# Kernel tuning notes

Measured on AMD Instinct MI355X. Metric: run time of the kernel, lower is better.

## Reference

```python
import jax, jax.numpy as jnp
import numpy as np

B, T, E, H, L, Q, FF, V, C = 4, 2048, 16, 4, 2, 16, 64, 32000, 16
D = E // H  # head_dim = 4


def pos_encoding(t, e):
    # Sinusoidal PE, matching torch: pe[:,0::2]=sin, pe[:,1::2]=cos
    pos = jnp.arange(t, dtype=jnp.float32)[:, None]
    div = jnp.exp(jnp.arange(0, e, 2, dtype=jnp.float32) * (-np.log(10000.0) / e))
    ang = pos * div  # [T, E/2]
    return jnp.stack([jnp.sin(ang), jnp.cos(ang)], axis=-1).reshape(t, e)


def setup_inputs() -> dict:
    key = jax.random.key(0)
    ks = jax.random.split(key, 12)
    def n(k, shape, scale=0.1):
        return (jax.random.normal(k, shape) * scale).astype(jnp.float32)
    return {
        "tokens": jax.random.randint(ks[0], (B, T), 0, V),
        "emb": n(ks[1], (V, E)),
        "Wq": n(ks[2], (L, E, E)), "Wk": n(ks[3], (L, E, E)),
        "Wv": n(ks[4], (L, E, E)), "Wo": n(ks[5], (L, E, E)),
        "theta": n(ks[6], (L, Q), 1.0),
        "W1": n(ks[7], (L, E, FF)), "b1": jnp.zeros((L, FF), jnp.float32),
        "W2": n(ks[8], (L, FF, E)), "b2": jnp.zeros((L, E), jnp.float32),
        "gamma": jnp.ones((E,), jnp.float32), "beta": jnp.zeros((E,), jnp.float32),
        "Wc": n(ks[9], (E, C)), "bc": jnp.zeros((C,), jnp.float32),
    }


def reference(tokens, emb, Wq, Wk, Wv, Wo, theta, W1, b1, W2, b2, gamma, beta, Wc, bc):
    x = emb[tokens] + pos_encoding(T, E)[None]  # [B,T,E]
    for l in range(L):  # fixed small layer count
        # --- multi-head self-attention (no mask, eval mode: dropout off) ---
        q = (x @ Wq[l]).reshape(B, T, H, D)
        k = (x @ Wk[l]).reshape(B, T, H, D)
        v = (x @ Wv[l]).reshape(B, T, H, D)
        scores = jnp.einsum('bqhd,bkhd->bhqk', q, k) / np.sqrt(D).astype(np.float32)
        attn = jax.nn.softmax(scores, axis=-1)  # [B,H,T,T]
        o = jnp.einsum('bhqk,bkhd->bqhd', attn, v).reshape(B, T, E) @ Wo[l]
        x = x + o
        # --- quantum feed-forward ---
        # RX(x_w)|0> then RY(theta_w), measure PauliZ per wire. Single-qubit
        # gates on a product state factorize exactly: <Z_w> = cos(theta_w)*cos(x_w)
        q_out = jnp.cos(theta[l]) * jnp.cos(x)  # [B,T,E]
        h = jax.nn.relu(q_out @ W1[l] + b1[l])
        x = x + (h @ W2[l] + b2[l])
    # final LayerNorm
    mu = x.mean(-1, keepdims=True)
    var = ((x - mu) ** 2).mean(-1, keepdims=True)
    x = (x - mu) / jnp.sqrt(var + 1e-5) * gamma + beta
    # mean pool over tokens + classifier
    return x.mean(axis=1) @ Wc + bc  # [B,C]
```

## Files before the change

### kernel.cpp

```cpp
#include <hip/hip_runtime.h>
#include <hip/hip_bf16.h>
#include <math.h>

#define B_ 4
#define T_ 2048
#define E_ 16
#define H_ 4
#define D_ 4
#define L_ 2
#define FF_ 64
#define C_ 16

#define QSCALE 0.7213475204444817f

typedef __hip_bfloat16 bf16;

#if __has_builtin(__builtin_amdgcn_exp2f)
__device__ __forceinline__ float fast_exp2(float x) { return __builtin_amdgcn_exp2f(x); }
#else
__device__ __forceinline__ float fast_exp2(float x) { return exp2f(x); }
#endif

__device__ __forceinline__ bool probe_bf16(const void* gamma) {
  return ((const unsigned*)gamma)[0] == 0x3F803F80u;
}
__device__ __forceinline__ float ldin(const void* p, int i, bool isb) {
  if (isb) {
    unsigned short u = ((const unsigned short*)p)[i];
    union { unsigned x; float f; } c; c.x = ((unsigned)u) << 16;
    return c.f;
  }
  return ((const float*)p)[i];
}
__device__ __forceinline__ void unpack2(unsigned u, float& a, float& b) {
  union { unsigned x; float f; } lo, hi;
  lo.x = u << 16; hi.x = u & 0xffff0000u;
  a = lo.f; b = hi.f;
}

__global__ __launch_bounds__(64) void embed_qkv_kernel(
    const int* __restrict__ tokens, const void* __restrict__ emb,
    const void* __restrict__ Wq, const void* __restrict__ Wk, const void* __restrict__ Wv,
    int wofs, const void* __restrict__ gamma,
    float* __restrict__ X, float* __restrict__ Qh, float* __restrict__ KV) {
  __shared__ float wq[256], wk[256], wv[256];
  bool isb = probe_bf16(gamma);
  int tid = threadIdx.x;
  #pragma unroll
  for (int i = tid; i < 256; i += 64) {
    wq[i] = ldin(Wq, wofs + i, isb);
    wk[i] = ldin(Wk, wofs + i, isb);
    wv[i] = ldin(Wv, wofs + i, isb);
  }
  int r = tid & 31, half = tid >> 5;
  int row = blockIdx.x * 32 + r;
  int t = row & (T_ - 1);
  int tok = tokens[row];
  float x[16];
  if (isb) {
    const unsigned short* eb = (const unsigned short*)emb + (size_t)tok * E_;
    uint4 e0 = ((const uint4*)eb)[0], e1 = ((const uint4*)eb)[1];
    unpack2(e0.x, x[0], x[1]);   unpack2(e0.y, x[2], x[3]);
    unpack2(e0.z, x[4], x[5]);   unpack2(e0.w, x[6], x[7]);
    unpack2(e1.x, x[8], x[9]);   unpack2(e1.y, x[10], x[11]);
    unpack2(e1.z, x[12], x[13]); unpack2(e1.w, x[14], x[15]);
  } else {
    const float* er = (const float*)emb + (size_t)tok * E_;
    #pragma unroll
    for (int i = 0; i < 4; i++) {
      float4 f = ((const float4*)er)[i];
      x[4*i+0] = f.x; x[4*i+1] = f.y; x[4*i+2] = f.z; x[4*i+3] = f.w;
    }
  }
  const float divs[8] = {1.f, 0.31622776601683794f, 0.1f, 0.031622776601683794f,
                         0.01f, 0.0031622776601683794f, 0.001f, 0.00031622776601683794f};
  #pragma unroll
  for (int i = 0; i < 8; i++) {
    float ang = (float)t * divs[i];
    x[2*i]   += __sinf(ang);
    x[2*i+1] += __cosf(ang);
  }
  __syncthreads();
  if (half == 0) {
    float* xr = X + (size_t)row * E_;
    #pragma unroll
    for (int i = 0; i < 4; i++)
      ((float4*)xr)[i] = make_float4(x[4*i], x[4*i+1], x[4*i+2], x[4*i+3]);
  }
  int b = row >> 11;
  #pragma unroll
  for (int hh = 0; hh < 2; hh++) {
    int h = half * 2 + hh;
    float q[4] = {0,0,0,0}, k[4] = {0,0,0,0}, v[4] = {0,0,0,0};
    #pragma unroll
    for (int e = 0; e < 16; e++) {
      float xv = x[e];
      #pragma unroll
      for (int d = 0; d < 4; d++) {
        q[d] = fmaf(xv, wq[e*16 + h*4 + d], q[d]);
        k[d] = fmaf(xv, wk[e*16 + h*4 + d], k[d]);
        v[d] = fmaf(xv, wv[e*16 + h*4 + d], v[d]);
      }
    }
    size_t bh = (size_t)(b * H_ + h);
    *(float4*)(Qh + (bh * T_ + t) * 4) =
        make_float4(q[0]*QSCALE, q[1]*QSCALE, q[2]*QSCALE, q[3]*QSCALE);
    float* kvp = KV + (bh * T_ + t) * 8;
    *(float4*)(kvp)     = make_float4(k[0], k[1], k[2], k[3]);
    *(float4*)(kvp + 4) = make_float4(v[0], v[1], v[2], v[3]);
  }
}

__global__ __launch_bounds__(1024) void attn_kernel(
    const float* __restrict__ Qh, const float* __restrict__ KV,
    float* __restrict__ Ob) {
  __shared__ float part[16][64][5];
  int blk = blockIdx.x;
  int bh = blk >> 5;
  int qc = blk & 31;
  int tid = threadIdx.x;
  int qi = tid & 63;
  int ks = __builtin_amdgcn_readfirstlane(tid >> 6);
  int t = qc * 64 + qi;
  float4 q = *(const float4*)(Qh + ((size_t)bh * T_ + t) * 4);
  const float4* kv4 = (const float4*)(KV + ((size_t)bh * T_ + ks * (T_/16)) * 8);
  float l = 0.f, ax = 0.f, ay = 0.f, az = 0.f, aw = 0.f;
  #pragma unroll 8
  for (int j = 0; j < T_/16; j++) {
    float4 k4 = kv4[2*j];
    float4 v4 = kv4[2*j+1];
    float s = fmaf(q.x, k4.x, fmaf(q.y, k4.y, fmaf(q.z, k4.z, q.w * k4.w)));
    float p = fast_exp2(s);
    l += p;
    ax = fmaf(p, v4.x, ax); ay = fmaf(p, v4.y, ay);
    az = fmaf(p, v4.z, az); aw = fmaf(p, v4.w, aw);
  }
  part[ks][qi][0] = ax; part[ks][qi][1] = ay;
  part[ks][qi][2] = az; part[ks][qi][3] = aw;
  part[ks][qi][4] = l;
  __syncthreads();
  if (tid < 64) {
    float sx = 0.f, sy = 0.f, sz = 0.f, sw = 0.f, sl = 0.f;
    #pragma unroll
    for (int w = 0; w < 16; w++) {
      sx += part[w][tid][0]; sy += part[w][tid][1];
      sz += part[w][tid][2]; sw += part[w][tid][3];
      sl += part[w][tid][4];
    }
    float inv = 1.f / sl;
    int b = bh >> 2, h = bh & 3;
    *(float4*)(Ob + ((size_t)b * T_ + qc * 64 + tid) * E_ + h * D_) =
        make_float4(sx * inv, sy * inv, sz * inv, sw * inv);
  }
}

__global__ __launch_bounds__(64) void opff_qkv_kernel(
    const float* __restrict__ Ob, const void* __restrict__ Wo, int wofs,
    const void* __restrict__ theta, const void* __restrict__ W1, const void* __restrict__ b1,
    const void* __restrict__ W2, const void* __restrict__ b2, int l,
    const void* __restrict__ Wq, const void* __restrict__ Wk, const void* __restrict__ Wv,
    int wofs2, int do_qkv,
    const void* __restrict__ gamma, float* __restrict__ X,
    float* __restrict__ Qh, float* __restrict__ KV) {
  __shared__ float wo[256], w1[E_*FF_], w2[FF_*E_], s1[FF_], s2[E_], ct[E_];
  __shared__ float wq[256], wk[256], wv[256];
  bool isb = probe_bf16(gamma);
  int tid = threadIdx.x;
  int o1 = l * E_ * FF_;
  #pragma unroll
  for (int i = tid; i < 256; i += 64) wo[i] = ldin(Wo, wofs + i, isb);
  #pragma unroll
  for (int i = tid; i < E_*FF_; i += 64) {
    w1[i] = ldin(W1, o1 + i, isb);
    w2[i] = ldin(W2, o1 + i, isb);
  }
  if (tid < FF_) s1[tid] = ldin(b1, l*FF_ + tid, isb);
  if (tid < E_) {
    s2[tid] = ldin(b2, l*E_ + tid, isb);
    ct[tid] = cosf(ldin(theta, l*E_ + tid, isb));
  }
  if (do_qkv) {
    #pragma unroll
    for (int i = tid; i < 256; i += 64) {
      wq[i] = ldin(Wq, wofs2 + i, isb);
      wk[i] = ldin(Wk, wofs2 + i, isb);
      wv[i] = ldin(Wv, wofs2 + i, isb);
    }
  }
  __syncthreads();
  int r = tid & 31;
  int half = tid >> 5;
  size_t row = (size_t)blockIdx.x * 32 + r;
  float* xr = X + row * E_;
  const float* orow = Ob + row * E_;
  float x[16], o[16];
  #pragma unroll
  for (int i = 0; i < 4; i++) {
    float4 f = ((const float4*)xr)[i];
    x[4*i]=f.x; x[4*i+1]=f.y; x[4*i+2]=f.z; x[4*i+3]=f.w;
    float4 g = ((const float4*)orow)[i];
    o[4*i]=g.x; o[4*i+1]=g.y; o[4*i+2]=g.z; o[4*i+3]=g.w;
  }
  #pragma unroll
  for (int c = 0; c < 16; c++) {
    float s = 0.f;
    #pragma unroll
    for (int e = 0; e < 16; e++) s = fmaf(o[e], wo[e*16 + c], s);
    x[c] += s;
  }
  float qo[16];
  #pragma unroll
  for (int e = 0; e < 16; e++) qo[e] = ct[e] * __cosf(x[e]);
  float acc[16];
  #pragma unroll
  for (int e = 0; e < 16; e++) acc[e] = (half == 0) ? s2[e] : 0.f;
  int j0 = half * 32;
  for (int j = j0; j < j0 + 32; j++) {
    float s = s1[j];
    #pragma unroll
    for (int e = 0; e < 16; e++) s = fmaf(qo[e], w1[e*FF_ + j], s);
    s = fmaxf(s, 0.f);
    #pragma unroll
    for (int e = 0; e < 16; e++) acc[e] = fmaf(s, w2[j*E_ + e], acc[e]);
  }
  #pragma unroll
  for (int e = 0; e < 16; e++) acc[e] += __shfl_xor(acc[e], 32, 64);
  #pragma unroll
  for (int e = 0; e < 16; e++) x[e] += acc[e];
  if (half == 0) {
    #pragma unroll
    for (int i = 0; i < 4; i++)
      ((float4*)xr)[i] = make_float4(x[4*i], x[4*i+1], x[4*i+2], x[4*i+3]);
  }
  if (do_qkv) {
    int b = (int)(row >> 11), t = (int)(row & (T_ - 1));
    #pragma unroll
    for (int hh = 0; hh < 2; hh++) {
      int h = half * 2 + hh;
      float q[4] = {0,0,0,0}, k[4] = {0,0,0,0}, v[4] = {0,0,0,0};
      #pragma unroll
      for (int e = 0; e < 16; e++) {
        float xv = x[e];
        #pragma unroll
        for (int d = 0; d < 4; d++) {
          q[d] = fmaf(xv, wq[e*16 + h*4 + d], q[d]);
          k[d] = fmaf(xv, wk[e*16 + h*4 + d], k[d]);
          v[d] = fmaf(xv, wv[e*16 + h*4 + d], v[d]);
        }
      }
      size_t bh = (size_t)(b * H_ + h);
      *(float4*)(Qh + (bh * T_ + t) * 4) =
          make_float4(q[0]*QSCALE, q[1]*QSCALE, q[2]*QSCALE, q[3]*QSCALE);
      float* kvp = KV + (bh * T_ + t) * 8;
      *(float4*)(kvp)     = make_float4(k[0], k[1], k[2], k[3]);
      *(float4*)(kvp + 4) = make_float4(v[0], v[1], v[2], v[3]);
    }
  }
}

__global__ __launch_bounds__(1024) void lnfin_kernel(
    const float* __restrict__ X, const void* __restrict__ gamma,
    const void* __restrict__ beta, const void* __restrict__ Wc,
    const void* __restrict__ bc, float* __restrict__ out) {
  __shared__ float sg[16], sb[16], wsum[16][16], pool[16];
  bool isb = probe_bf16(gamma);
  int tid = threadIdx.x;
  int b = blockIdx.x;
  if (tid < 16) { sg[tid] = ldin(gamma, tid, isb); sb[tid] = ldin(beta, tid, isb); }
  __syncthreads();
  float acc[16];
  #pragma unroll
  for (int e = 0; e < 16; e++) acc[e] = 0.f;
  #pragma unroll
  for (int rr = 0; rr < 2; rr++) {
    int r = tid + rr * 1024;
    const float* xr = X + ((size_t)b * T_ + r) * E_;
    float x[16];
    #pragma unroll
    for (int i = 0; i < 4; i++) {
      float4 f = ((const float4*)xr)[i];
      x[4*i]=f.x; x[4*i+1]=f.y; x[4*i+2]=f.z; x[4*i+3]=f.w;
    }
    float mu = 0.f;
    #pragma unroll
    for (int e = 0; e < 16; e++) mu += x[e];
    mu *= (1.f/16.f);
    float var = 0.f;
    #pragma unroll
    for (int e = 0; e < 16; e++) { float d = x[e]-mu; var = fmaf(d, d, var); }
    var *= (1.f/16.f);
    float inv = rsqrtf(var + 1e-5f);
    #pragma unroll
    for (int e = 0; e < 16; e++) acc[e] += (x[e]-mu)*inv*sg[e] + sb[e];
  }
  #pragma unroll
  for (int e = 0; e < 16; e++) {
    float s = acc[e];
    #pragma unroll
    for (int m = 1; m < 64; m <<= 1) s += __shfl_xor(s, m, 64);
    acc[e] = s;
  }
  int wid = tid >> 6;
  if ((tid & 63) == 0) {
    #pragma unroll
    for (int e = 0; e < 16; e++) wsum[wid][e] = acc[e];
  }
  __syncthreads();
  if (tid < 16) {
    float s = 0.f;
    #pragma unroll
    for (int w = 0; w < 16; w++) s += wsum[w][tid];
    pool[tid] = s * (1.f / T_);
  }
  __syncthreads();
  if (tid < 16) {
    float a = ldin(bc, tid, isb);
    #pragma unroll
    for (int e = 0; e < 16; e++) a = fmaf(pool[e], ldin(Wc, e*16 + tid, isb), a);
    out[b * 16 + tid] = a;
  }
}

extern "C" void kernel_launch(void* const* d_in, const int* in_sizes, int n_in,
                              void* d_out, int out_size, void* d_ws, size_t ws_size,
                              hipStream_t stream) {
  const int*  tokens = (const int*)d_in[0];
  const void* emb    = d_in[1];
  const void* Wq     = d_in[2];
  const void* Wk     = d_in[3];
  const void* Wv     = d_in[4];
  const void* Wo     = d_in[5];
  const void* theta  = d_in[6];
  const void* W1     = d_in[7];
  const void* b1     = d_in[8];
  const void* W2     = d_in[9];
  const void* b2     = d_in[10];
  const void* gamma  = d_in[11];
  const void* beta   = d_in[12];
  const void* Wc     = d_in[13];
  const void* bc     = d_in[14];

  float* ws = (float*)d_ws;
  float* X   = ws;
  float* Qh  = ws + 131072;
  float* KV  = ws + 262144;
  float* Ob  = ws + 524288;
  float* out = (float*)d_out;

  embed_qkv_kernel<<<256, 64, 0, stream>>>(tokens, emb, Wq, Wk, Wv, 0, gamma,
                                           X, Qh, KV);
  for (int l = 0; l < L_; l++) {
    attn_kernel<<<B_*H_*(T_/64), 1024, 0, stream>>>(Qh, KV, Ob);
    int wofs = l * E_ * E_;
    int wofs2 = (l + 1) * E_ * E_;
    int do_qkv = (l + 1 < L_) ? 1 : 0;
    opff_qkv_kernel<<<256, 64, 0, stream>>>(Ob, Wo, wofs, theta, W1, b1, W2, b2, l,
                                            Wq, Wk, Wv, wofs2, do_qkv,
                                            gamma, X, Qh, KV);
  }
  lnfin_kernel<<<B_, 1024, 0, stream>>>(X, gamma, beta, Wc, bc, out);
}
```

Baseline: 90.25 us.

## Compute attention scores with fp16 MFMA and split Q/K/V storage

The attention kernel now computes QK^T scores with the 16x16x32 fp16 MFMA instruction instead of scalar FMAs. Q and K are stored as fp16 and V stays fp32 in separate arrays, and blocks are restructured into 256 threads covering 32 queries with a two-way key split. Partial sums are reduced with cross-lane shuffles plus a small shared-memory combine. The K dimension of 4 is zero-padded to 32, so most of each MFMA does no useful work. The per-lane exp and PV accumulation are still scalar, and fp16 Q/K lowers score precision.

```diff
diff --git a/kernel.cpp b/kernel.cpp
--- a/kernel.cpp
+++ b/kernel.cpp
@@ -14,6 +14,8 @@
 #define QSCALE 0.7213475204444817f
 
 typedef __hip_bfloat16 bf16;
+typedef _Float16 h8 __attribute__((ext_vector_type(8)));
+typedef float f4 __attribute__((ext_vector_type(4)));
 
 #if __has_builtin(__builtin_amdgcn_exp2f)
 __device__ __forceinline__ float fast_exp2(float x) { return __builtin_amdgcn_exp2f(x); }
@@ -21,6 +23,14 @@
 __device__ __forceinline__ float fast_exp2(float x) { return exp2f(x); }
 #endif
 
+__device__ __forceinline__ unsigned short f2h(float f) {
+  _Float16 h = (_Float16)f;
+  return __builtin_bit_cast(unsigned short, h);
+}
+__device__ __forceinline__ _Float16 h2(unsigned short u) {
+  return __builtin_bit_cast(_Float16, u);
+}
+
 __device__ __forceinline__ bool probe_bf16(const void* gamma) {
   return ((const unsigned*)gamma)[0] == 0x3F803F80u;
 }
@@ -42,7 +52,8 @@
     const int* __restrict__ tokens, const void* __restrict__ emb,
     const void* __restrict__ Wq, const void* __restrict__ Wk, const void* __restrict__ Wv,
     int wofs, const void* __restrict__ gamma,
-    float* __restrict__ X, float* __restrict__ Qh, float* __restrict__ KV) {
+    float* __restrict__ X, ushort4* __restrict__ Qhp, ushort4* __restrict__ Khp,
+    float4* __restrict__ Vfp) {
   __shared__ float wq[256], wk[256], wv[256];
   bool isb = probe_bf16(gamma);
   int tid = threadIdx.x;
@@ -102,55 +113,82 @@
         v[d] = fmaf(xv, wv[e*16 + h*4 + d], v[d]);
       }
     }
-    size_t bh = (size_t)(b * H_ + h);
-    *(float4*)(Qh + (bh * T_ + t) * 4) =
-        make_float4(q[0]*QSCALE, q[1]*QSCALE, q[2]*QSCALE, q[3]*QSCALE);
-    float* kvp = KV + (bh * T_ + t) * 8;
-    *(float4*)(kvp)     = make_float4(k[0], k[1], k[2], k[3]);
-    *(float4*)(kvp + 4) = make_float4(v[0], v[1], v[2], v[3]);
-  }
-}
-
-__global__ __launch_bounds__(1024) void attn_kernel(
-    const float* __restrict__ Qh, const float* __restrict__ KV,
-    float* __restrict__ Ob) {
-  __shared__ float part[16][64][5];
+    size_t idx = (size_t)(b * H_ + h) * T_ + t;
+    Qhp[idx] = make_ushort4(f2h(q[0]*QSCALE), f2h(q[1]*QSCALE),
+                            f2h(q[2]*QSCALE), f2h(q[3]*QSCALE));
+    Khp[idx] = make_ushort4(f2h(k[0]), f2h(k[1]), f2h(k[2]), f2h(k[3]));
+    Vfp[idx] = make_float4(v[0], v[1], v[2], v[3]);
+  }
+}
+
+__global__ __launch_bounds__(256) void attn_kernel(
+    const ushort4* __restrict__ Qhp, const ushort4* __restrict__ Khp,
+    const float4* __restrict__ Vfp, float* __restrict__ Ob) {
+  __shared__ float part[2][2][4][20];
   int blk = blockIdx.x;
-  int bh = blk >> 5;
-  int qc = blk & 31;
+  int bh = blk >> 6;
+  int qp = blk & 63;
   int tid = threadIdx.x;
-  int qi = tid & 63;
-  int ks = __builtin_amdgcn_readfirstlane(tid >> 6);
-  int t = qc * 64 + qi;
-  float4 q = *(const float4*)(Qh + ((size_t)bh * T_ + t) * 4);
-  const float4* kv4 = (const float4*)(KV + ((size_t)bh * T_ + ks * (T_/16)) * 8);
-  float l = 0.f, ax = 0.f, ay = 0.f, az = 0.f, aw = 0.f;
-  #pragma unroll 8
-  for (int j = 0; j < T_/16; j++) {
-    float4 k4 = kv4[2*j];
-    float4 v4 = kv4[2*j+1];
-    float s = fmaf(q.x, k4.x, fmaf(q.y, k4.y, fmaf(q.z, k4.z, q.w * k4.w)));
-    float p = fast_exp2(s);
-    l += p;
-    ax = fmaf(p, v4.x, ax); ay = fmaf(p, v4.y, ay);
-    az = fmaf(p, v4.z, az); aw = fmaf(p, v4.w, aw);
-  }
-  part[ks][qi][0] = ax; part[ks][qi][1] = ay;
-  part[ks][qi][2] = az; part[ks][qi][3] = aw;
-  part[ks][qi][4] = l;
-  __syncthreads();
-  if (tid < 64) {
-    float sx = 0.f, sy = 0.f, sz = 0.f, sw = 0.f, sl = 0.f;
-    #pragma unroll
-    for (int w = 0; w < 16; w++) {
-      sx += part[w][tid][0]; sy += part[w][tid][1];
-      sz += part[w][tid][2]; sw += part[w][tid][3];
-      sl += part[w][tid][4];
-    }
-    float inv = 1.f / sl;
+  int lane = tid & 63;
+  int w = tid >> 6;
+  int qt_l = w >> 1;
+  int ks = w & 1;
+  int qbase = qp * 32 + qt_l * 16;
+  int kl = lane & 15;
+  size_t bhT = (size_t)bh * T_;
+  const _Float16 z = (_Float16)0.f;
+  ushort4 qv = make_ushort4(0, 0, 0, 0);
+  if (lane < 16) qv = Qhp[bhT + qbase + lane];
+  h8 afrag = {h2(qv.x), h2(qv.y), h2(qv.z), h2(qv.w), z, z, z, z};
+  f4 zero4 = {0.f, 0.f, 0.f, 0.f};
+  float o[4][4] = {{0,0,0,0},{0,0,0,0},{0,0,0,0},{0,0,0,0}};
+  float lr[4] = {0,0,0,0};
+  int kt0 = ks * 64;
+  #pragma unroll 4
+  for (int kt = kt0; kt < kt0 + 64; kt++) {
+    ushort4 kv = Khp[bhT + kt*16 + kl];
+    if (lane >= 16) kv = make_ushort4(0, 0, 0, 0);
+    h8 bfrag = {h2(kv.x), h2(kv.y), h2(kv.z), h2(kv.w), z, z, z, z};
+    f4 sc = __builtin_amdgcn_mfma_f32_16x16x32_f16(afrag, bfrag, zero4, 0, 0, 0);
+    float4 v = Vfp[bhT + kt*16 + kl];
+    float p0 = fast_exp2(sc[0]), p1 = fast_exp2(sc[1]);
+    float p2 = fast_exp2(sc[2]), p3 = fast_exp2(sc[3]);
+    lr[0] += p0; lr[1] += p1; lr[2] += p2; lr[3] += p3;
+    o[0][0] = fmaf(p0, v.x, o[0][0]); o[0][1] = fmaf(p0, v.y, o[0][1]);
+    o[0][2] = fmaf(p0, v.z, o[0][2]); o[0][3] = fmaf(p0, v.w, o[0][3]);
+    o[1][0] = fmaf(p1, v.x, o[1][0]); o[1][1] = fmaf(p1, v.y, o[1][1]);
+    o[1][2] = fmaf(p1, v.z, o[1][2]); o[1][3] = fmaf(p1, v.w, o[1][3]);
+    o[2][0] = fmaf(p2, v.x, o[2][0]); o[2][1] = fmaf(p2, v.y, o[2][1]);
+    o[2][2] = fmaf(p2, v.z, o[2][2]); o[2][3] = fmaf(p2, v.w, o[2][3]);
+    o[3][0] = fmaf(p3, v.x, o[3][0]); o[3][1] = fmaf(p3, v.y, o[3][1]);
+    o[3][2] = fmaf(p3, v.z, o[3][2]); o[3][3] = fmaf(p3, v.w, o[3][3]);
+  }
+  #pragma unroll
+  for (int m = 1; m < 16; m <<= 1) {
+    #pragma unroll
+    for (int r = 0; r < 4; r++) {
+      lr[r] += __shfl_xor(lr[r], m, 64);
+      #pragma unroll
+      for (int d = 0; d < 4; d++) o[r][d] += __shfl_xor(o[r][d], m, 64);
+    }
+  }
+  if ((lane & 15) == 0) {
+    float* pp = &part[qt_l][ks][lane >> 4][0];
+    #pragma unroll
+    for (int r = 0; r < 4; r++) {
+      #pragma unroll
+      for (int d = 0; d < 4; d++) pp[r*4 + d] = o[r][d];
+      pp[16 + r] = lr[r];
+    }
+  }
+  __syncthreads();
+  if (tid < 128) {
+    int qt = tid >> 6, zz = tid & 63, q = zz >> 2, d = zz & 3;
+    int g = q >> 2, r = q & 3;
+    float ov = part[qt][0][g][r*4 + d] + part[qt][1][g][r*4 + d];
+    float ls = part[qt][0][g][16 + r] + part[qt][1][g][16 + r];
     int b = bh >> 2, h = bh & 3;
-    *(float4*)(Ob + ((size_t)b * T_ + qc * 64 + tid) * E_ + h * D_) =
-        make_float4(sx * inv, sy * inv, sz * inv, sw * inv);
+    Ob[((size_t)b * T_ + qp*32 + qt*16 + q) * E_ + h*4 + d] = ov / ls;
   }
 }
 
@@ -161,7 +199,7 @@
     const void* __restrict__ Wq, const void* __restrict__ Wk, const void* __restrict__ Wv,
     int wofs2, int do_qkv,
     const void* __restrict__ gamma, float* __restrict__ X,
-    float* __restrict__ Qh, float* __restrict__ KV) {
+    ushort4* __restrict__ Qhp, ushort4* __restrict__ Khp, float4* __restrict__ Vfp) {
   __shared__ float wo[256], w1[E_*FF_], w2[FF_*E_], s1[FF_], s2[E_], ct[E_];
   __shared__ float wq[256], wk[256], wv[256];
   bool isb = probe_bf16(gamma);
@@ -248,12 +286,11 @@
           v[d] = fmaf(xv, wv[e*16 + h*4 + d], v[d]);
         }
       }
-      size_t bh = (size_t)(b * H_ + h);
-      *(float4*)(Qh + (bh * T_ + t) * 4) =
-          make_float4(q[0]*QSCALE, q[1]*QSCALE, q[2]*QSCALE, q[3]*QSCALE);
-      float* kvp = KV + (bh * T_ + t) * 8;
-      *(float4*)(kvp)     = make_float4(k[0], k[1], k[2], k[3]);
-      *(float4*)(kvp + 4) = make_float4(v[0], v[1], v[2], v[3]);
+      size_t idx = (size_t)(b * H_ + h) * T_ + t;
+      Qhp[idx] = make_ushort4(f2h(q[0]*QSCALE), f2h(q[1]*QSCALE),
+                              f2h(q[2]*QSCALE), f2h(q[3]*QSCALE));
+      Khp[idx] = make_ushort4(f2h(k[0]), f2h(k[1]), f2h(k[2]), f2h(k[3]));
+      Vfp[idx] = make_float4(v[0], v[1], v[2], v[3]);
     }
   }
 }
@@ -341,22 +378,23 @@
   const void* bc     = d_in[14];
 
   float* ws = (float*)d_ws;
-  float* X   = ws;
-  float* Qh  = ws + 131072;
-  float* KV  = ws + 262144;
-  float* Ob  = ws + 524288;
+  float*   X   = ws;
+  ushort4* Qhp = (ushort4*)(ws + 131072);
+  ushort4* Khp = (ushort4*)(ws + 196608);
+  float4*  Vfp = (float4*)(ws + 262144);
+  float*   Ob  = ws + 393216;
   float* out = (float*)d_out;
 
   embed_qkv_kernel<<<256, 64, 0, stream>>>(tokens, emb, Wq, Wk, Wv, 0, gamma,
-                                           X, Qh, KV);
+                                           X, Qhp, Khp, Vfp);
   for (int l = 0; l < L_; l++) {
-    attn_kernel<<<B_*H_*(T_/64), 1024, 0, stream>>>(Qh, KV, Ob);
+    attn_kernel<<<16*64, 256, 0, stream>>>(Qhp, Khp, Vfp, Ob);
     int wofs = l * E_ * E_;
     int wofs2 = (l + 1) * E_ * E_;
     int do_qkv = (l + 1 < L_) ? 1 : 0;
     opff_qkv_kernel<<<256, 64, 0, stream>>>(Ob, Wo, wofs, theta, W1, b1, W2, b2, l,
                                             Wq, Wk, Wv, wofs2, do_qkv,
-                                            gamma, X, Qh, KV);
+                                            gamma, X, Qhp, Khp, Vfp);
   }
   lnfin_kernel<<<B_, 1024, 0, stream>>>(X, gamma, beta, Wc, bc, out);
 }
```

After: 95.43 us. 5.7% more time.
